# Performance work log

Measured on AMD Instinct MI355X. Metric: run time of the kernel, lower is better.

## Reference

```python
import jax, jax.numpy as jnp
import numpy as np
import math

N = 50000      # nodes
E = 800000     # edges (avg degree 16)
T = 4          # time steps
F = 64         # feature dim (in = hidden = out)
MAX_LEN = 200  # positional encoding table length
EPS = 1e-5     # BatchNorm eps


def _make_pe(time_dim, max_len):
    pe = np.zeros((max_len, time_dim), dtype=np.float32)
    position = np.arange(max_len, dtype=np.float32)[:, None]
    div_term = np.exp(np.arange(0, time_dim, 2, dtype=np.float32) * (-math.log(10000.0) / time_dim))
    pe[:, 0::2] = np.sin(position * div_term)
    pe[:, 1::2] = np.cos(position * div_term)
    return jnp.asarray(pe)


def setup_inputs() -> dict:
    key = jax.random.key(0)
    ks = jax.random.split(key, 10)
    xav = math.sqrt(2.0 / (F + F))  # xavier_normal_ std for square linear
    return {
        "node_features": jax.random.normal(ks[0], (N, T, F), dtype=jnp.float32),
        "edges_weight": jax.random.uniform(ks[1], (T, E), dtype=jnp.float32),
        "identities": jax.random.randint(ks[2], (T,), 0, MAX_LEN),
        "edge_src": jax.random.randint(ks[3], (E,), 0, N),
        "edge_dst": jax.random.randint(ks[4], (E,), 0, N),
        "pe": _make_pe(F, MAX_LEN),
        "W0": jax.random.normal(ks[5], (F, F), dtype=jnp.float32) * xav,
        "W1": jax.random.normal(ks[6], (F, F), dtype=jnp.float32) * xav,
        "g0": jnp.ones((F,), jnp.float32),
        "b0": jnp.zeros((F,), jnp.float32),
        "g1": jnp.ones((F,), jnp.float32),
        "b1": jnp.zeros((F,), jnp.float32),
    }


def _gcn_layer(h, ew, edge_src, edge_dst, W):
    # gather-mul-scatter: msg_e = h[src_e] * w_e ; agg_v = sum_{e: dst=v} msg_e
    msg = h[edge_src] * ew                                   # (E, T, F)
    agg = jax.ops.segment_sum(msg, edge_dst, num_segments=N)  # (N, T, F)
    readout = agg.mean(axis=0)                                # dgl.mean_nodes (single graph) -> (T, F)
    return agg @ W, readout @ W


def _batchnorm(x, gamma, beta):
    # training-mode batch stats over all non-channel dims
    mean = x.mean(axis=(0, 1))
    var = x.var(axis=(0, 1))
    return (x - mean) * jax.lax.rsqrt(var + EPS) * gamma + beta


def reference(node_features, edges_weight, identities, edge_src, edge_dst,
              pe, W0, W1, g0, b0, g1, b1):
    # positional encoding added per time step
    h = node_features + pe[identities]          # (N, T, F)
    ew = edges_weight.T[:, :, None]             # (E, T, 1)
    # layer 0: gcn -> dropout(eval=identity) -> BN -> ReLU
    h, readout = _gcn_layer(h, ew, edge_src, edge_dst, W0)
    h = jax.nn.relu(_batchnorm(h, g0, b0))
    # layer 1 (output layer)
    h, readout = _gcn_layer(h, ew, edge_src, edge_dst, W1)
    h = jax.nn.relu(_batchnorm(h, g1, b1))
    return h, readout
```

## Files before the change

kernel.cpp:

```cpp
#include <hip/hip_runtime.h>

#define TF 256

typedef __attribute__((ext_vector_type(8))) short short8;
typedef __attribute__((ext_vector_type(4))) float f32x4;
typedef __attribute__((ext_vector_type(4))) unsigned int uint4v;

__device__ inline unsigned short f2bf(float x) {
  unsigned u = __float_as_uint(x);
  u += 0x7fffu + ((u >> 16) & 1u);
  return (unsigned short)(u >> 16);
}
__device__ inline unsigned pack2(unsigned short lo, unsigned short hi) {
  return (unsigned)lo | ((unsigned)hi << 16);
}
__device__ inline float bflo(unsigned u) { return __uint_as_float(u << 16); }
__device__ inline float bfhi(unsigned u) { return __uint_as_float(u & 0xffff0000u); }

__global__ void hist_kernel(const int* __restrict__ dst, int* __restrict__ indeg, int E) {
  int e = blockIdx.x * blockDim.x + threadIdx.x;
  if (e < E) atomicAdd(&indeg[dst[e]], 1);
}

__global__ __launch_bounds__(1024) void scan_part1(const int* __restrict__ indeg,
                                                   int* __restrict__ partials, int n) {
  __shared__ int wsum[16];
  const int tid = threadIdx.x;
  const int lane = tid & 63;
  const int wid = tid >> 6;
  int i = blockIdx.x * 1024 + tid;
  int s = (i < n) ? indeg[i] : 0;
  #pragma unroll
  for (int o = 1; o < 64; o <<= 1) s += __shfl_xor(s, o, 64);
  if (lane == 0) wsum[wid] = s;
  __syncthreads();
  if (tid == 0) {
    int acc = 0;
    #pragma unroll
    for (int w = 0; w < 16; ++w) acc += wsum[w];
    partials[blockIdx.x] = acc;
  }
}

__global__ __launch_bounds__(64) void scan_part2(const int* __restrict__ partials,
                                                 int* __restrict__ base,
                                                 int* __restrict__ offsets, int nb, int n) {
  const int i = threadIdx.x;
  int v = (i < nb) ? partials[i] : 0;
  int s = v;
  #pragma unroll
  for (int o = 1; o < 64; o <<= 1) {
    int t = __shfl_up(s, o, 64);
    if (i >= o) s += t;
  }
  if (i < nb) base[i] = s - v;
  if (i == nb - 1) offsets[n] = s;
}

__global__ __launch_bounds__(1024) void scan_part3(const int* __restrict__ indeg,
                                                   const int* __restrict__ base,
                                                   int* __restrict__ offsets,
                                                   int* __restrict__ cursor, int n) {
  __shared__ int wsum[16];
  const int tid = threadIdx.x;
  const int lane = tid & 63;
  const int wid = tid >> 6;
  int i = blockIdx.x * 1024 + tid;
  int v = (i < n) ? indeg[i] : 0;
  int s = v;
  #pragma unroll
  for (int o = 1; o < 64; o <<= 1) {
    int t = __shfl_up(s, o, 64);
    if (lane >= o) s += t;
  }
  if (lane == 63) wsum[wid] = s;
  __syncthreads();
  if (tid == 0) {
    int acc = 0;
    #pragma unroll
    for (int w = 0; w < 16; ++w) { int t = wsum[w]; wsum[w] = acc; acc += t; }
  }
  __syncthreads();
  int excl = s - v + wsum[wid] + base[blockIdx.x];
  if (i < n) { offsets[i] = excl; cursor[i] = excl; }
}

__global__ void fill_kernel(const int* __restrict__ src, const int* __restrict__ dst,
                            const float* __restrict__ ew, int* __restrict__ cursor,
                            uint4v* __restrict__ csr_ent, int E) {
  int e = blockIdx.x * blockDim.x + threadIdx.x;
  if (e >= E) return;
  int d = dst[e];
  int pos = atomicAdd(&cursor[d], 1);
  uint4v ent;
  ent.x = (unsigned)(src[e] << 9);
  ent.y = pack2(f2bf(ew[e]), f2bf(ew[(size_t)E + e]));
  ent.z = pack2(f2bf(ew[2 * (size_t)E + e]), f2bf(ew[3 * (size_t)E + e]));
  ent.w = 0u;
  __builtin_nontemporal_store(ent, &csr_ent[pos]);
}

__global__ void prep_kernel(const float* __restrict__ x, const float* __restrict__ pe,
                            const int* __restrict__ ids, uint2* __restrict__ h0, int n4) {
  int i = blockIdx.x * blockDim.x + threadIdx.x;
  const int stride = gridDim.x * blockDim.x;
  for (; i < n4; i += stride) {
    int e0 = (i << 2) & (TF - 1);
    int t = e0 >> 6;
    int f4 = e0 & 63;
    float4 v = reinterpret_cast<const float4*>(x)[i];
    float4 p = *reinterpret_cast<const float4*>(&pe[ids[t] * 64 + f4]);
    uint2 o;
    o.x = pack2(f2bf(v.x + p.x), f2bf(v.y + p.y));
    o.y = pack2(f2bf(v.z + p.z), f2bf(v.w + p.w));
    h0[i] = o;
  }
}

template <int LAYER>
__global__ __launch_bounds__(256) void aggregate_kernel(
    const char* __restrict__ h_base, const int* __restrict__ offsets,
    const uint4* __restrict__ csr_ent,
    const float* __restrict__ scale, const float* __restrict__ shiftv,
    uint4* __restrict__ agg, int n_nodes) {
  const int lane = threadIdx.x & 63;
  const int wid = threadIdx.x >> 6;
  const int v = blockIdx.x * 4 + wid;
  if (v >= n_nodes) return;
  const int p = lane >> 5;
  const unsigned q = lane & 31;
  const unsigned qb = q << 4;
  const int tw = q >> 3;

  float sc[8], sh[8];
  if (LAYER == 1) {
    const int f0 = (q & 7) << 3;
    #pragma unroll
    for (int j = 0; j < 8; ++j) { sc[j] = scale[f0 + j]; sh[j] = shiftv[f0 + j]; }
  }

  float acc[8];
  #pragma unroll
  for (int j = 0; j < 8; ++j) acc[j] = 0.f;

  auto wext = [&](uint4 ent) -> float {
    unsigned word = (tw & 2) ? ent.z : ent.y;
    return (tw & 1) ? bfhi(word) : bflo(word);
  };
  auto body = [&](uint4 u, float w) {
    float x[8] = {bflo(u.x), bfhi(u.x), bflo(u.y), bfhi(u.y),
                  bflo(u.z), bfhi(u.z), bflo(u.w), bfhi(u.w)};
    #pragma unroll
    for (int j = 0; j < 8; ++j) {
      float t = x[j];
      if (LAYER == 1) t = fmaxf(0.f, fmaf(t, sc[j], sh[j]));
      acc[j] = fmaf(w, t, acc[j]);
    }
  };

  const int beg = offsets[v];
  const int end = offsets[v + 1];
  int i = beg;
  for (; i + 8 <= end; i += 8) {
    uint4 ent[4];
    #pragma unroll
    for (int c = 0; c < 4; ++c) ent[c] = csr_ent[i + 2 * c + p];
    uint4 row[4];
    #pragma unroll
    for (int c = 0; c < 4; ++c)
      row[c] = *reinterpret_cast<const uint4*>(h_base + (ent[c].x + qb));
    #pragma unroll
    for (int c = 0; c < 4; ++c) body(row[c], wext(ent[c]));
  }
  for (; i + 2 <= end; i += 2) {
    const uint4 ent = csr_ent[i + p];
    const uint4 row = *reinterpret_cast<const uint4*>(h_base + (ent.x + qb));
    body(row, wext(ent));
  }
  if (i < end) {
    const uint4 ent = csr_ent[i];
    const uint4 row = *reinterpret_cast<const uint4*>(h_base + (ent.x + qb));
    body(row, p == 0 ? wext(ent) : 0.f);
  }

  #pragma unroll
  for (int j = 0; j < 8; ++j) acc[j] += __shfl_xor(acc[j], 32, 64);
  if (lane < 32) {
    uint4 o;
    o.x = pack2(f2bf(acc[0]), f2bf(acc[1]));
    o.y = pack2(f2bf(acc[2]), f2bf(acc[3]));
    o.z = pack2(f2bf(acc[4]), f2bf(acc[5]));
    o.w = pack2(f2bf(acc[6]), f2bf(acc[7]));
    agg[(size_t)v * 32 + q] = o;
  }
}

__global__ __launch_bounds__(512) void wfrag_kernel(const float* __restrict__ W0,
                                                    const float* __restrict__ W1,
                                                    short* __restrict__ wf0,
                                                    short* __restrict__ wf1) {
  const int frag = threadIdx.x >> 6, lane = threadIdx.x & 63;
  const int c = frag >> 1, h = frag & 1;
  const int n = (c << 4) + (lane & 15);
  const int k0 = h * 32 + ((lane >> 4) << 3);
  short* o0 = wf0 + frag * 512 + lane * 8;
  short* o1 = wf1 + frag * 512 + lane * 8;
  #pragma unroll
  for (int i = 0; i < 8; ++i) {
    o0[i] = (short)f2bf(W0[(k0 + i) * 64 + n]);
    o1[i] = (short)f2bf(W1[(k0 + i) * 64 + n]);
  }
}

__global__ __launch_bounds__(256) void mfma_matmul_kernel(
    const unsigned short* __restrict__ aggb, const short* __restrict__ wf,
    unsigned short* __restrict__ y_bf, float* __restrict__ part, int R) {
  const int tid = threadIdx.x;
  const int lane = tid & 63;
  const int wid = tid >> 6;

  short8 bfr[8];
  #pragma unroll
  for (int g = 0; g < 8; ++g)
    bfr[g] = *reinterpret_cast<const short8*>(wf + g * 512 + lane * 8);

  f32x4 csum[4];
  float ssq[4];
  #pragma unroll
  for (int c = 0; c < 4; ++c) { csum[c] = (f32x4){0.f, 0.f, 0.f, 0.f}; ssq[c] = 0.f; }

  const int nrb = (R + 15) >> 4;
  const int k0 = (lane >> 4) << 3;
  for (int rb = blockIdx.x * 4 + wid; rb < nrb; rb += gridDim.x * 4) {
    const int base = rb << 4;
    const int row = base + (lane & 15);
    short8 a0 = (short8){0, 0, 0, 0, 0, 0, 0, 0};
    short8 a1 = a0;
    if (row < R) {
      const short8* ap = reinterpret_cast<const short8*>(aggb + (size_t)row * 64 + k0);
      a0 = ap[0];
      a1 = ap[4];
    }
    f32x4 acc[4];
    #pragma unroll
    for (int c = 0; c < 4; ++c) {
      acc[c] = (f32x4){0.f, 0.f, 0.f, 0.f};
      acc[c] = __builtin_amdgcn_mfma_f32_16x16x32_bf16(a0, bfr[c * 2 + 0], acc[c], 0, 0, 0);
      acc[c] = __builtin_amdgcn_mfma_f32_16x16x32_bf16(a1, bfr[c * 2 + 1], acc[c], 0, 0, 0);
    }
    const int rbase = base + ((lane >> 4) << 2);
    #pragma unroll
    for (int c = 0; c < 4; ++c) {
      const int col = (c << 4) + (lane & 15);
      #pragma unroll
      for (int i = 0; i < 4; ++i) {
        const int r2 = rbase + i;
        if (r2 < R) {
          const float val = acc[c][i];
          y_bf[(size_t)r2 * 64 + col] = f2bf(val);
          csum[c][i] += val;
          ssq[c] += val * val;
        }
      }
    }
  }

  #pragma unroll
  for (int c = 0; c < 4; ++c) {
    #pragma unroll
    for (int i = 0; i < 4; ++i) {
      float v = csum[c][i];
      v += __shfl_xor(v, 16, 64);
      v += __shfl_xor(v, 32, 64);
      csum[c][i] = v;
    }
    float q = ssq[c];
    q += __shfl_xor(q, 16, 64);
    q += __shfl_xor(q, 32, 64);
    ssq[c] = q;
  }
  __shared__ float lcs[4][256];
  __shared__ float lsq[4][64];
  if (lane < 16) {
    #pragma unroll
    for (int c = 0; c < 4; ++c) {
      #pragma unroll
      for (int i = 0; i < 4; ++i) lcs[wid][i * 64 + (c << 4) + lane] = csum[c][i];
      lsq[wid][(c << 4) + lane] = ssq[c];
    }
  }
  __syncthreads();
  float s = lcs[0][tid] + lcs[1][tid] + lcs[2][tid] + lcs[3][tid];
  part[(size_t)blockIdx.x * 320 + tid] = s;
  if (tid < 64)
    part[(size_t)blockIdx.x * 320 + 256 + tid] =
        lsq[0][tid] + lsq[1][tid] + lsq[2][tid] + lsq[3][tid];
}

__global__ __launch_bounds__(1024) void reduce_part_kernel(const float* __restrict__ part,
                                                           float* __restrict__ red, int nblk) {
  __shared__ float lds[1024];
  const int tid = threadIdx.x;
  const int col = blockIdx.x * 16 + (tid & 15);
  const int r = tid >> 4;
  float s = 0.f;
  for (int bk = r; bk < nblk; bk += 64) s += part[(size_t)bk * 320 + col];
  lds[tid] = s;
  __syncthreads();
  #pragma unroll
  for (int off = 512; off >= 16; off >>= 1) {
    if (tid < off) lds[tid] += lds[tid + off];
    __syncthreads();
  }
  if (tid < 16) red[col] = lds[tid];
}

__global__ __launch_bounds__(64) void bn_from_red_kernel(
    const float* __restrict__ red, const float* __restrict__ g, const float* __restrict__ b,
    float* __restrict__ scale, float* __restrict__ shiftv, float inv_count) {
  const int f = threadIdx.x;
  float sum = red[f] + red[64 + f] + red[128 + f] + red[192 + f];
  float mean = sum * inv_count;
  float var = red[256 + f] * inv_count - mean * mean;
  float sc = g[f] * rsqrtf(var + 1e-5f);
  scale[f] = sc;
  shiftv[f] = fmaf(-mean, sc, b[f]);
}

__global__ __launch_bounds__(256) void finalize_from_red_kernel(
    const float* __restrict__ red, const float* __restrict__ g, const float* __restrict__ b,
    float* __restrict__ scale, float* __restrict__ shiftv, float inv_count,
    float* __restrict__ out_readout, float invN) {
  const int tid = threadIdx.x;
  out_readout[tid] = red[tid] * invN;
  if (tid < 64) {
    float sum = red[tid] + red[64 + tid] + red[128 + tid] + red[192 + tid];
    float mean = sum * inv_count;
    float var = red[256 + tid] * inv_count - mean * mean;
    float sc = g[tid] * rsqrtf(var + 1e-5f);
    scale[tid] = sc;
    shiftv[tid] = fmaf(-mean, sc, b[tid]);
  }
}

__global__ void bn_relu_out_kernel(const uint4* __restrict__ yb,
                                   const float* __restrict__ scale,
                                   const float* __restrict__ shiftv,
                                   float4* __restrict__ out, int n8) {
  int i = blockIdx.x * blockDim.x + threadIdx.x;
  if (i >= n8) return;
  const int f0 = (i & 7) << 3;
  uint4 u = yb[i];
  float x[8] = {bflo(u.x), bfhi(u.x), bflo(u.y), bfhi(u.y),
                bflo(u.z), bfhi(u.z), bflo(u.w), bfhi(u.w)};
  float4 o0, o1;
  o0.x = fmaxf(0.f, fmaf(x[0], scale[f0 + 0], shiftv[f0 + 0]));
  o0.y = fmaxf(0.f, fmaf(x[1], scale[f0 + 1], shiftv[f0 + 1]));
  o0.z = fmaxf(0.f, fmaf(x[2], scale[f0 + 2], shiftv[f0 + 2]));
  o0.w = fmaxf(0.f, fmaf(x[3], scale[f0 + 3], shiftv[f0 + 3]));
  o1.x = fmaxf(0.f, fmaf(x[4], scale[f0 + 4], shiftv[f0 + 4]));
  o1.y = fmaxf(0.f, fmaf(x[5], scale[f0 + 5], shiftv[f0 + 5]));
  o1.z = fmaxf(0.f, fmaf(x[6], scale[f0 + 6], shiftv[f0 + 6]));
  o1.w = fmaxf(0.f, fmaf(x[7], scale[f0 + 7], shiftv[f0 + 7]));
  out[i * 2 + 0] = o0;
  out[i * 2 + 1] = o1;
}

extern "C" void kernel_launch(void* const* d_in, const int* in_sizes, int n_in,
                              void* d_out, int out_size, void* d_ws, size_t ws_size,
                              hipStream_t stream) {
  const float* node_features = (const float*)d_in[0];
  const float* edges_weight  = (const float*)d_in[1];
  const int*   identities    = (const int*)d_in[2];
  const int*   edge_src      = (const int*)d_in[3];
  const int*   edge_dst      = (const int*)d_in[4];
  const float* pe            = (const float*)d_in[5];
  const float* W0            = (const float*)d_in[6];
  const float* W1            = (const float*)d_in[7];
  const float* g0            = (const float*)d_in[8];
  const float* b0            = (const float*)d_in[9];
  const float* g1            = (const float*)d_in[10];
  const float* b1            = (const float*)d_in[11];

  const int T = in_sizes[2];
  const int E = in_sizes[3];
  const int F = in_sizes[8];
  const int N = in_sizes[0] / (T * F);
  const int R = N * T;

  float* out = (float*)d_out;
  float* out_h = out;
  float* out_readout = out + (size_t)N * T * F;

  char* ws = (char*)d_ws;
  size_t off = 0;
  auto alloc = [&](size_t bytes) -> void* {
    off = (off + 255) & ~(size_t)255;
    void* p = ws + off;
    off += bytes;
    return p;
  };
  int*    indeg    = (int*)alloc((size_t)N * sizeof(int));
  int*    partials = (int*)alloc(64 * sizeof(int));
  int*    base_    = (int*)alloc(64 * sizeof(int));
  int*    offsets  = (int*)alloc(((size_t)N + 1) * sizeof(int));
  int*    cursor   = (int*)alloc((size_t)N * sizeof(int));
  uint4v* csr_ent  = (uint4v*)alloc((size_t)E * 16);
  unsigned short* h0b  = (unsigned short*)alloc((size_t)N * TF * 2);
  unsigned short* aggb = (unsigned short*)alloc((size_t)N * TF * 2);
  short* wf0 = (short*)alloc(8 * 512 * sizeof(short));
  short* wf1 = (short*)alloc(8 * 512 * sizeof(short));
  const int MMB = 256;
  float* mm_part = (float*)alloc((size_t)MMB * 320 * sizeof(float));
  float* red     = (float*)alloc(320 * sizeof(float));
  float* scale0 = (float*)alloc(64 * sizeof(float));
  float* shift0 = (float*)alloc(64 * sizeof(float));
  float* scale1 = (float*)alloc(64 * sizeof(float));
  float* shift1 = (float*)alloc(64 * sizeof(float));
  (void)ws_size;

  const int nb = (N + 1023) / 1024;

  hipMemsetAsync(indeg, 0, (size_t)N * sizeof(int), stream);
  hipLaunchKernelGGL(hist_kernel, dim3((E + 255) / 256), dim3(256), 0, stream, edge_dst, indeg, E);
  hipLaunchKernelGGL(scan_part1, dim3(nb), dim3(1024), 0, stream, indeg, partials, N);
  hipLaunchKernelGGL(scan_part2, dim3(1), dim3(64), 0, stream, partials, base_, offsets, nb, N);
  hipLaunchKernelGGL(scan_part3, dim3(nb), dim3(1024), 0, stream, indeg, base_, offsets, cursor, N);
  hipLaunchKernelGGL(fill_kernel, dim3((E + 255) / 256), dim3(256), 0, stream,
                     edge_src, edge_dst, edges_weight, cursor, csr_ent, E);

  hipLaunchKernelGGL(wfrag_kernel, dim3(1), dim3(512), 0, stream, W0, W1, wf0, wf1);
  hipLaunchKernelGGL(prep_kernel, dim3(2048), dim3(256), 0, stream,
                     node_features, pe, identities, (uint2*)h0b, (N * TF) / 4);

  const int agg_blocks = (N + 3) / 4;

  hipLaunchKernelGGL((aggregate_kernel<0>), dim3(agg_blocks), dim3(256), 0, stream,
                     (const char*)h0b, offsets, (const uint4*)csr_ent,
                     nullptr, nullptr, (uint4*)aggb, N);
  hipLaunchKernelGGL(mfma_matmul_kernel, dim3(MMB), dim3(256), 0, stream,
                     aggb, wf0, h0b , mm_part, R);
  hipLaunchKernelGGL(reduce_part_kernel, dim3(20), dim3(1024), 0, stream, mm_part, red, MMB);
  hipLaunchKernelGGL(bn_from_red_kernel, dim3(1), dim3(64), 0, stream,
                     red, g0, b0, scale0, shift0, 1.0f / (float)R);

  hipLaunchKernelGGL((aggregate_kernel<1>), dim3(agg_blocks), dim3(256), 0, stream,
                     (const char*)h0b , offsets, (const uint4*)csr_ent,
                     scale0, shift0, (uint4*)aggb, N);
  hipLaunchKernelGGL(mfma_matmul_kernel, dim3(MMB), dim3(256), 0, stream,
                     aggb, wf1, h0b , mm_part, R);
  hipLaunchKernelGGL(reduce_part_kernel, dim3(20), dim3(1024), 0, stream, mm_part, red, MMB);
  hipLaunchKernelGGL(finalize_from_red_kernel, dim3(1), dim3(256), 0, stream,
                     red, g1, b1, scale1, shift1, 1.0f / (float)R,
                     out_readout, 1.0f / (float)N);

  hipLaunchKernelGGL(bn_relu_out_kernel, dim3((R * 8 + 255) / 256), dim3(256), 0, stream,
                     (const uint4*)h0b, scale1, shift1, (float4*)out_h, R * 8);
}
```

Before: 288.9 us.

## Fuse prep with histogram, merge scan with weight prep, prefetch CSR entries, nontemporal memory ops

Merges the feature prep and in-degree histogram into one grid-stride kernel, and folds the weight-fragment conversion into the single-block scan kernel, removing two launches. The aggregation loop is software-pipelined so the next group of CSR entries is loaded while the current gathered rows are accumulated. Nontemporal loads and stores are applied across streaming buffers, and the matmul grid is doubled. Nontemporal hints on csr_ent and aggb, which are reused later, could lower cache hit rates between layers.

```diff
diff --git a/kernel.cpp b/kernel.cpp
--- a/kernel.cpp
+++ b/kernel.cpp
@@ -5,6 +5,7 @@
 typedef __attribute__((ext_vector_type(8))) short short8;
 typedef __attribute__((ext_vector_type(4))) float f32x4;
 typedef __attribute__((ext_vector_type(4))) unsigned int uint4v;
+typedef __attribute__((ext_vector_type(2))) unsigned int uint2v;
 
 __device__ inline unsigned short f2bf(float x) {
   unsigned u = __float_as_uint(x);
@@ -17,9 +18,25 @@
 __device__ inline float bflo(unsigned u) { return __uint_as_float(u << 16); }
 __device__ inline float bfhi(unsigned u) { return __uint_as_float(u & 0xffff0000u); }
 
-__global__ void hist_kernel(const int* __restrict__ dst, int* __restrict__ indeg, int E) {
-  int e = blockIdx.x * blockDim.x + threadIdx.x;
-  if (e < E) atomicAdd(&indeg[dst[e]], 1);
+__global__ void prep_hist_kernel(const float* __restrict__ x, const float* __restrict__ pe,
+                                 const int* __restrict__ ids, uint2v* __restrict__ h0, int n4,
+                                 const int* __restrict__ dst, int* __restrict__ indeg, int E) {
+  const int gid = blockIdx.x * blockDim.x + threadIdx.x;
+  const int stride = gridDim.x * blockDim.x;
+  for (int i = gid; i < n4; i += stride) {
+    int e0 = (i << 2) & (TF - 1);
+    int t = e0 >> 6;
+    int f4 = e0 & 63;
+    f32x4 v = __builtin_nontemporal_load(&reinterpret_cast<const f32x4*>(x)[i]);
+    const f32x4 p = *reinterpret_cast<const f32x4*>(&pe[ids[t] * 64 + f4]);
+    uint2v o;
+    o.x = pack2(f2bf(v.x + p.x), f2bf(v.y + p.y));
+    o.y = pack2(f2bf(v.z + p.z), f2bf(v.w + p.w));
+    h0[i] = o;
+  }
+  for (int e = gid; e < E; e += stride) {
+    atomicAdd(&indeg[__builtin_nontemporal_load(&dst[e])], 1);
+  }
 }
 
 __global__ __launch_bounds__(1024) void scan_part1(const int* __restrict__ indeg,
@@ -42,19 +59,33 @@
   }
 }
 
-__global__ __launch_bounds__(64) void scan_part2(const int* __restrict__ partials,
-                                                 int* __restrict__ base,
-                                                 int* __restrict__ offsets, int nb, int n) {
-  const int i = threadIdx.x;
-  int v = (i < nb) ? partials[i] : 0;
-  int s = v;
-  #pragma unroll
-  for (int o = 1; o < 64; o <<= 1) {
-    int t = __shfl_up(s, o, 64);
-    if (i >= o) s += t;
-  }
-  if (i < nb) base[i] = s - v;
-  if (i == nb - 1) offsets[n] = s;
+__global__ __launch_bounds__(512) void scan2_wfrag_kernel(
+    const int* __restrict__ partials, int* __restrict__ base, int* __restrict__ offsets,
+    int nb, int n, const float* __restrict__ W0, const float* __restrict__ W1,
+    short* __restrict__ wf0, short* __restrict__ wf1) {
+  const int tid = threadIdx.x;
+  if (tid < 64) {
+    int v = (tid < nb) ? partials[tid] : 0;
+    int s = v;
+    #pragma unroll
+    for (int o = 1; o < 64; o <<= 1) {
+      int t = __shfl_up(s, o, 64);
+      if (tid >= o) s += t;
+    }
+    if (tid < nb) base[tid] = s - v;
+    if (tid == nb - 1) offsets[n] = s;
+  }
+  const int frag = tid >> 6, lane = tid & 63;
+  const int c = frag >> 1, h = frag & 1;
+  const int col = (c << 4) + (lane & 15);
+  const int k0 = h * 32 + ((lane >> 4) << 3);
+  short* o0 = wf0 + frag * 512 + lane * 8;
+  short* o1 = wf1 + frag * 512 + lane * 8;
+  #pragma unroll
+  for (int i = 0; i < 8; ++i) {
+    o0[i] = (short)f2bf(W0[(k0 + i) * 64 + col]);
+    o1[i] = (short)f2bf(W1[(k0 + i) * 64 + col]);
+  }
 }
 
 __global__ __launch_bounds__(1024) void scan_part3(const int* __restrict__ indeg,
@@ -90,39 +121,26 @@
                             uint4v* __restrict__ csr_ent, int E) {
   int e = blockIdx.x * blockDim.x + threadIdx.x;
   if (e >= E) return;
-  int d = dst[e];
+  int d = __builtin_nontemporal_load(&dst[e]);
   int pos = atomicAdd(&cursor[d], 1);
   uint4v ent;
-  ent.x = (unsigned)(src[e] << 9);
-  ent.y = pack2(f2bf(ew[e]), f2bf(ew[(size_t)E + e]));
-  ent.z = pack2(f2bf(ew[2 * (size_t)E + e]), f2bf(ew[3 * (size_t)E + e]));
+  ent.x = (unsigned)(__builtin_nontemporal_load(&src[e]) << 9);
+  float w0 = __builtin_nontemporal_load(&ew[e]);
+  float w1 = __builtin_nontemporal_load(&ew[(size_t)E + e]);
+  float w2 = __builtin_nontemporal_load(&ew[2 * (size_t)E + e]);
+  float w3 = __builtin_nontemporal_load(&ew[3 * (size_t)E + e]);
+  ent.y = pack2(f2bf(w0), f2bf(w1));
+  ent.z = pack2(f2bf(w2), f2bf(w3));
   ent.w = 0u;
   __builtin_nontemporal_store(ent, &csr_ent[pos]);
-}
-
-__global__ void prep_kernel(const float* __restrict__ x, const float* __restrict__ pe,
-                            const int* __restrict__ ids, uint2* __restrict__ h0, int n4) {
-  int i = blockIdx.x * blockDim.x + threadIdx.x;
-  const int stride = gridDim.x * blockDim.x;
-  for (; i < n4; i += stride) {
-    int e0 = (i << 2) & (TF - 1);
-    int t = e0 >> 6;
-    int f4 = e0 & 63;
-    float4 v = reinterpret_cast<const float4*>(x)[i];
-    float4 p = *reinterpret_cast<const float4*>(&pe[ids[t] * 64 + f4]);
-    uint2 o;
-    o.x = pack2(f2bf(v.x + p.x), f2bf(v.y + p.y));
-    o.y = pack2(f2bf(v.z + p.z), f2bf(v.w + p.w));
-    h0[i] = o;
-  }
 }
 
 template <int LAYER>
 __global__ __launch_bounds__(256) void aggregate_kernel(
     const char* __restrict__ h_base, const int* __restrict__ offsets,
-    const uint4* __restrict__ csr_ent,
+    const uint4v* __restrict__ csr_ent,
     const float* __restrict__ scale, const float* __restrict__ shiftv,
-    uint4* __restrict__ agg, int n_nodes) {
+    uint4v* __restrict__ agg, int n_nodes) {
   const int lane = threadIdx.x & 63;
   const int wid = threadIdx.x >> 6;
   const int v = blockIdx.x * 4 + wid;
@@ -143,11 +161,11 @@
   #pragma unroll
   for (int j = 0; j < 8; ++j) acc[j] = 0.f;
 
-  auto wext = [&](uint4 ent) -> float {
+  auto wext = [&](uint4v ent) -> float {
     unsigned word = (tw & 2) ? ent.z : ent.y;
     return (tw & 1) ? bfhi(word) : bflo(word);
   };
-  auto body = [&](uint4 u, float w) {
+  auto body = [&](uint4v u, float w) {
     float x[8] = {bflo(u.x), bfhi(u.x), bflo(u.y), bfhi(u.y),
                   bflo(u.z), bfhi(u.z), bflo(u.w), bfhi(u.w)};
     #pragma unroll
@@ -161,54 +179,52 @@
   const int beg = offsets[v];
   const int end = offsets[v + 1];
   int i = beg;
-  for (; i + 8 <= end; i += 8) {
-    uint4 ent[4];
-    #pragma unroll
-    for (int c = 0; c < 4; ++c) ent[c] = csr_ent[i + 2 * c + p];
-    uint4 row[4];
-    #pragma unroll
-    for (int c = 0; c < 4; ++c)
-      row[c] = *reinterpret_cast<const uint4*>(h_base + (ent[c].x + qb));
-    #pragma unroll
-    for (int c = 0; c < 4; ++c) body(row[c], wext(ent[c]));
+  if (i + 8 <= end) {
+    uint4v e0 = __builtin_nontemporal_load(&csr_ent[i + p]);
+    uint4v e1 = __builtin_nontemporal_load(&csr_ent[i + 2 + p]);
+    uint4v e2 = __builtin_nontemporal_load(&csr_ent[i + 4 + p]);
+    uint4v e3 = __builtin_nontemporal_load(&csr_ent[i + 6 + p]);
+    for (;;) {
+      const uint4v r0 = *reinterpret_cast<const uint4v*>(h_base + (e0.x + qb));
+      const uint4v r1 = *reinterpret_cast<const uint4v*>(h_base + (e1.x + qb));
+      const uint4v r2 = *reinterpret_cast<const uint4v*>(h_base + (e2.x + qb));
+      const uint4v r3 = *reinterpret_cast<const uint4v*>(h_base + (e3.x + qb));
+      const float w0 = wext(e0), w1 = wext(e1), w2 = wext(e2), w3 = wext(e3);
+      i += 8;
+      const bool more = (i + 8 <= end);
+      if (more) {
+        e0 = __builtin_nontemporal_load(&csr_ent[i + p]);
+        e1 = __builtin_nontemporal_load(&csr_ent[i + 2 + p]);
+        e2 = __builtin_nontemporal_load(&csr_ent[i + 4 + p]);
+        e3 = __builtin_nontemporal_load(&csr_ent[i + 6 + p]);
+      }
+      body(r0, w0);
+      body(r1, w1);
+      body(r2, w2);
+      body(r3, w3);
+      if (!more) break;
+    }
   }
   for (; i + 2 <= end; i += 2) {
-    const uint4 ent = csr_ent[i + p];
-    const uint4 row = *reinterpret_cast<const uint4*>(h_base + (ent.x + qb));
+    const uint4v ent = __builtin_nontemporal_load(&csr_ent[i + p]);
+    const uint4v row = *reinterpret_cast<const uint4v*>(h_base + (ent.x + qb));
     body(row, wext(ent));
   }
   if (i < end) {
-    const uint4 ent = csr_ent[i];
-    const uint4 row = *reinterpret_cast<const uint4*>(h_base + (ent.x + qb));
+    const uint4v ent = __builtin_nontemporal_load(&csr_ent[i]);
+    const uint4v row = *reinterpret_cast<const uint4v*>(h_base + (ent.x + qb));
     body(row, p == 0 ? wext(ent) : 0.f);
   }
 
   #pragma unroll
   for (int j = 0; j < 8; ++j) acc[j] += __shfl_xor(acc[j], 32, 64);
   if (lane < 32) {
-    uint4 o;
+    uint4v o;
     o.x = pack2(f2bf(acc[0]), f2bf(acc[1]));
     o.y = pack2(f2bf(acc[2]), f2bf(acc[3]));
     o.z = pack2(f2bf(acc[4]), f2bf(acc[5]));
     o.w = pack2(f2bf(acc[6]), f2bf(acc[7]));
-    agg[(size_t)v * 32 + q] = o;
-  }
-}
-
-__global__ __launch_bounds__(512) void wfrag_kernel(const float* __restrict__ W0,
-                                                    const float* __restrict__ W1,
-                                                    short* __restrict__ wf0,
-                                                    short* __restrict__ wf1) {
-  const int frag = threadIdx.x >> 6, lane = threadIdx.x & 63;
-  const int c = frag >> 1, h = frag & 1;
-  const int n = (c << 4) + (lane & 15);
-  const int k0 = h * 32 + ((lane >> 4) << 3);
-  short* o0 = wf0 + frag * 512 + lane * 8;
-  short* o1 = wf1 + frag * 512 + lane * 8;
-  #pragma unroll
-  for (int i = 0; i < 8; ++i) {
-    o0[i] = (short)f2bf(W0[(k0 + i) * 64 + n]);
-    o1[i] = (short)f2bf(W1[(k0 + i) * 64 + n]);
+    __builtin_nontemporal_store(o, &agg[(size_t)v * 32 + q]);
   }
 }
 
@@ -238,8 +254,8 @@
     short8 a1 = a0;
     if (row < R) {
       const short8* ap = reinterpret_cast<const short8*>(aggb + (size_t)row * 64 + k0);
-      a0 = ap[0];
-      a1 = ap[4];
+      a0 = __builtin_nontemporal_load(ap);
+      a1 = __builtin_nontemporal_load(ap + 4);
     }
     f32x4 acc[4];
     #pragma unroll
@@ -343,17 +359,17 @@
   }
 }
 
-__global__ void bn_relu_out_kernel(const uint4* __restrict__ yb,
+__global__ void bn_relu_out_kernel(const uint4v* __restrict__ yb,
                                    const float* __restrict__ scale,
                                    const float* __restrict__ shiftv,
-                                   float4* __restrict__ out, int n8) {
+                                   f32x4* __restrict__ out, int n8) {
   int i = blockIdx.x * blockDim.x + threadIdx.x;
   if (i >= n8) return;
   const int f0 = (i & 7) << 3;
-  uint4 u = yb[i];
+  uint4v u = __builtin_nontemporal_load(&yb[i]);
   float x[8] = {bflo(u.x), bfhi(u.x), bflo(u.y), bfhi(u.y),
                 bflo(u.z), bfhi(u.z), bflo(u.w), bfhi(u.w)};
-  float4 o0, o1;
+  f32x4 o0, o1;
   o0.x = fmaxf(0.f, fmaf(x[0], scale[f0 + 0], shiftv[f0 + 0]));
   o0.y = fmaxf(0.f, fmaf(x[1], scale[f0 + 1], shiftv[f0 + 1]));
   o0.z = fmaxf(0.f, fmaf(x[2], scale[f0 + 2], shiftv[f0 + 2]));
@@ -362,8 +378,8 @@
   o1.y = fmaxf(0.f, fmaf(x[5], scale[f0 + 5], shiftv[f0 + 5]));
   o1.z = fmaxf(0.f, fmaf(x[6], scale[f0 + 6], shiftv[f0 + 6]));
   o1.w = fmaxf(0.f, fmaf(x[7], scale[f0 + 7], shiftv[f0 + 7]));
-  out[i * 2 + 0] = o0;
-  out[i * 2 + 1] = o1;
+  __builtin_nontemporal_store(o0, &out[i * 2 + 0]);
+  __builtin_nontemporal_store(o1, &out[i * 2 + 1]);
 }
 
 extern "C" void kernel_launch(void* const* d_in, const int* in_sizes, int n_in,
@@ -405,12 +421,12 @@
   int*    base_    = (int*)alloc(64 * sizeof(int));
   int*    offsets  = (int*)alloc(((size_t)N + 1) * sizeof(int));
   int*    cursor   = (int*)alloc((size_t)N * sizeof(int));
-  uint4v* csr_ent  = (uint4v*)alloc((size_t)E * 16);
+  uint4v* csr_ent  = (uint4v*)alloc(((size_t)E + 16) * 16);
   unsigned short* h0b  = (unsigned short*)alloc((size_t)N * TF * 2);
   unsigned short* aggb = (unsigned short*)alloc((size_t)N * TF * 2);
   short* wf0 = (short*)alloc(8 * 512 * sizeof(short));
   short* wf1 = (short*)alloc(8 * 512 * sizeof(short));
-  const int MMB = 256;
+  const int MMB = 512;
   float* mm_part = (float*)alloc((size_t)MMB * 320 * sizeof(float));
   float* red     = (float*)alloc(320 * sizeof(float));
   float* scale0 = (float*)alloc(64 * sizeof(float));
@@ -421,23 +437,22 @@
 
   const int nb = (N + 1023) / 1024;
 
-  hipMemsetAsync(indeg, 0, (size_t)N * sizeof(int), stream);
-  hipLaunchKernelGGL(hist_kernel, dim3((E + 255) / 256), dim3(256), 0, stream, edge_dst, indeg, E);
+  (void)hipMemsetAsync(indeg, 0, (size_t)N * sizeof(int), stream);
+  hipLaunchKernelGGL(prep_hist_kernel, dim3(2048), dim3(256), 0, stream,
+                     node_features, pe, identities, (uint2v*)h0b, (N * TF) / 4,
+                     edge_dst, indeg, E);
   hipLaunchKernelGGL(scan_part1, dim3(nb), dim3(1024), 0, stream, indeg, partials, N);
-  hipLaunchKernelGGL(scan_part2, dim3(1), dim3(64), 0, stream, partials, base_, offsets, nb, N);
+  hipLaunchKernelGGL(scan2_wfrag_kernel, dim3(1), dim3(512), 0, stream,
+                     partials, base_, offsets, nb, N, W0, W1, wf0, wf1);
   hipLaunchKernelGGL(scan_part3, dim3(nb), dim3(1024), 0, stream, indeg, base_, offsets, cursor, N);
   hipLaunchKernelGGL(fill_kernel, dim3((E + 255) / 256), dim3(256), 0, stream,
                      edge_src, edge_dst, edges_weight, cursor, csr_ent, E);
 
-  hipLaunchKernelGGL(wfrag_kernel, dim3(1), dim3(512), 0, stream, W0, W1, wf0, wf1);
-  hipLaunchKernelGGL(prep_kernel, dim3(2048), dim3(256), 0, stream,
-                     node_features, pe, identities, (uint2*)h0b, (N * TF) / 4);
-
   const int agg_blocks = (N + 3) / 4;
 
   hipLaunchKernelGGL((aggregate_kernel<0>), dim3(agg_blocks), dim3(256), 0, stream,
-                     (const char*)h0b, offsets, (const uint4*)csr_ent,
-                     nullptr, nullptr, (uint4*)aggb, N);
+                     (const char*)h0b, offsets, csr_ent,
+                     nullptr, nullptr, (uint4v*)aggb, N);
   hipLaunchKernelGGL(mfma_matmul_kernel, dim3(MMB), dim3(256), 0, stream,
                      aggb, wf0, h0b , mm_part, R);
   hipLaunchKernelGGL(reduce_part_kernel, dim3(20), dim3(1024), 0, stream, mm_part, red, MMB);
@@ -445,8 +460,8 @@
                      red, g0, b0, scale0, shift0, 1.0f / (float)R);
 
   hipLaunchKernelGGL((aggregate_kernel<1>), dim3(agg_blocks), dim3(256), 0, stream,
-                     (const char*)h0b , offsets, (const uint4*)csr_ent,
-                     scale0, shift0, (uint4*)aggb, N);
+                     (const char*)h0b , offsets, csr_ent,
+                     scale0, shift0, (uint4v*)aggb, N);
   hipLaunchKernelGGL(mfma_matmul_kernel, dim3(MMB), dim3(256), 0, stream,
                      aggb, wf1, h0b , mm_part, R);
   hipLaunchKernelGGL(reduce_part_kernel, dim3(20), dim3(1024), 0, stream, mm_part, red, MMB);
@@ -455,5 +470,5 @@
                      out_readout, 1.0f / (float)N);
 
   hipLaunchKernelGGL(bn_relu_out_kernel, dim3((R * 8 + 255) / 256), dim3(256), 0, stream,
-                     (const uint4*)h0b, scale1, shift1, (float4*)out_h, R * 8);
-}
+                     (const uint4v*)h0b, scale1, shift1, (f32x4*)out_h, R * 8);
+}
```

Measured after the change: 300.0 us. 1.04x slower.
